# Kernel tuning notes

Measured on AMD Instinct MI355X. Metric: run time of the kernel, lower is better.

Reference implementation:

```python
import jax, jax.numpy as jnp
import numpy as np

KERNEL_SIZE = 4
SCALE = 0.5


def setup_inputs() -> dict:
    key = jax.random.key(0)
    k1, k2, k3 = jax.random.split(key, 3)
    M, K, N = 16384, 1024, 4096
    x = jax.random.normal(k1, (M, K), dtype=jnp.float32)
    weight = jax.random.normal(k2, (N, K), dtype=jnp.float32)
    bias = jax.random.normal(k3, (N,), dtype=jnp.float32)
    return {"x": x, "weight": weight, "bias": bias}


def reference(x, weight, bias):
    # y = x @ W^T + b : (M, N)
    y = jnp.einsum('mk,nk->mn', x, weight) + bias[None, :]
    M, N = y.shape
    valid_n = (N // KERNEL_SIZE) * KERNEL_SIZE
    # MaxPool1d(kernel_size, stride=kernel_size): (M, N//k, k) -> max over window
    pooled = jnp.max(y[:, :valid_n].reshape(M, valid_n // KERNEL_SIZE, KERNEL_SIZE), axis=-1)
    # sum over pooled features, then scale -> (M,)
    return jnp.sum(pooled, axis=-1) * SCALE
```

## Files before the change

### kernel.cpp

```cpp
#include <hip/hip_runtime.h>
#include <stdint.h>

#define M_DIM 16384
#define K_DIM 1024
#define N_DIM 4096
#define BM 128
#define BN 128
#define LDSP 40

#define TILE_ELEMS (128 * K_DIM)
#define SLAB_ELEMS (128 * 32)
#define NSLAB_X ((M_DIM / 128) * 32)
#define NSLAB_W ((N_DIM / 128) * 32)
#define CROW 20

typedef __bf16 bf16;
typedef __attribute__((ext_vector_type(8))) __bf16 bf16x8;
typedef __attribute__((ext_vector_type(4))) float f32x4;

__device__ __forceinline__ uint32_t pack2_bf16(float a, float b) {
    uint32_t ua = __float_as_uint(a);
    uint32_t ub = __float_as_uint(b);
    ua += 0x7fffu + ((ua >> 16) & 1u);
    ub += 0x7fffu + ((ub >> 16) & 1u);
    return (ua >> 16) | (ub & 0xffff0000u);
}

__global__ __launch_bounds__(256) void convert_pack_kernel(
    const float* __restrict__ x, const float* __restrict__ w,
    bf16* __restrict__ xp, bf16* __restrict__ wp)
{
    int slab = blockIdx.x;
    const float* src;
    bf16* dst;
    if (slab < NSLAB_X) { src = x; dst = xp; }
    else                { slab -= NSLAB_X; src = w; dst = wp; }
    const int tile = slab >> 5;
    const int s    = slab & 31;

    __shared__ uint32_t ls[128 * CROW];

    const int t = threadIdx.x;
    {
        const int r  = t >> 1;
        const int kh = (t & 1) * 16;
        const float4* p = (const float4*)(src + (size_t)(tile * 128 + r) * K_DIM + s * 32 + kh);
        float4 a = p[0], b = p[1], c = p[2], d = p[3];
        uint4* lp = (uint4*)&ls[r * CROW + (t & 1) * 8];
        uint4 v0, v1;
        v0.x = pack2_bf16(a.x, a.y); v0.y = pack2_bf16(a.z, a.w);
        v0.z = pack2_bf16(b.x, b.y); v0.w = pack2_bf16(b.z, b.w);
        v1.x = pack2_bf16(c.x, c.y); v1.y = pack2_bf16(c.z, c.w);
        v1.z = pack2_bf16(d.x, d.y); v1.w = pack2_bf16(d.z, d.w);
        lp[0] = v0; lp[1] = v1;
    }
    __syncthreads();
    uint4* dst4 = (uint4*)(dst + (size_t)tile * TILE_ELEMS + (size_t)s * SLAB_ELEMS);
    #pragma unroll
    for (int p = 0; p < 2; ++p) {
        const int c    = t + p * 256;
        const int lane = c & 63;
        const int rb   = c >> 6;
        const int q    = lane >> 4;
        const int lrow = lane & 15;
        const int r    = rb * 16 + lrow;
        const uint4* lp = (const uint4*)&ls[r * CROW + q * 4];
        dst4[c] = lp[0];
    }
}

__device__ __forceinline__ void load_set(const bf16* g, bf16x8* f) {
    #pragma unroll
    for (int i = 0; i < 4; ++i) f[i] = *(const bf16x8*)(g + i * 512);
}

__device__ __forceinline__ void do_mfma(const bf16x8* af, const bf16x8* bf,
                                        f32x4 acc[4][4]) {
    #pragma unroll
    for (int i = 0; i < 4; ++i)
        #pragma unroll
        for (int j = 0; j < 4; ++j)
            acc[i][j] = __builtin_amdgcn_mfma_f32_16x16x32_bf16(af[i], bf[j], acc[i][j], 0, 0, 0);
}

__global__ __launch_bounds__(256, 3) void gemm_pool_direct_kernel(
    const bf16* __restrict__ xp, const bf16* __restrict__ wp,
    const float* __restrict__ bias, float* __restrict__ out)
{
    const int b     = blockIdx.x;
    const int xcd   = b & 7;
    const int o     = (b >> 3) & 7;
    const int bx    = (b >> 6) & 31;
    const int phase = b >> 11;
    const int by    = phase * 64 + xcd * 8 + o;

    const int lane = threadIdx.x & 63;
    const int wave = threadIdx.x >> 6;
    const int wm = wave >> 1;
    const int wn = wave & 1;
    const int lr = lane & 15;
    const int quad = lane >> 4;

    const bf16* Abase = xp + (size_t)by * TILE_ELEMS + (wm * 4) * 512 + lane * 8;
    const bf16* Bbase = wp + (size_t)bx * TILE_ELEMS + (wn * 4) * 512 + lane * 8;

    f32x4 acc[4][4] = {};
    bf16x8 Af[2][4];
    bf16x8 Bf[3][4];

    load_set(Bbase, Bf[0]);
    load_set(Bbase + SLAB_ELEMS, Bf[1]);
    load_set(Abase, Af[0]);

    #pragma unroll
    for (int s = 0; s < 32; ++s) {
        if (s + 2 < 32) load_set(Bbase + (s + 2) * SLAB_ELEMS, Bf[(s + 2) % 3]);
        if (s + 1 < 32) load_set(Abase + (s + 1) * SLAB_ELEMS, Af[(s + 1) & 1]);
        do_mfma(Af[s & 1], Bf[s % 3], acc);
    }

    float bv[4];
    #pragma unroll
    for (int j = 0; j < 4; ++j)
        bv[j] = bias[bx * BN + wn * 64 + j * 16 + lr];

    #pragma unroll
    for (int i = 0; i < 4; ++i) {
        float rs[4] = {0.f, 0.f, 0.f, 0.f};
        #pragma unroll
        for (int j = 0; j < 4; ++j) {
            #pragma unroll
            for (int r = 0; r < 4; ++r) {
                float t = acc[i][j][r] + bv[j];
                t = fmaxf(t, __shfl_xor(t, 1, 64));
                t = fmaxf(t, __shfl_xor(t, 2, 64));
                rs[r] += t;
            }
        }
        #pragma unroll
        for (int r = 0; r < 4; ++r) {
            rs[r] += __shfl_xor(rs[r], 4, 64);
            rs[r] += __shfl_xor(rs[r], 8, 64);
        }
        if (lr == 0) {
            const int row = by * BM + wm * 64 + i * 16 + quad * 4;
            #pragma unroll
            for (int r = 0; r < 4; ++r)
                atomicAdd(&out[row + r], rs[r] * 0.5f);
        }
    }
}

__global__ __launch_bounds__(256) void fused_linear_pool_kernel(
    const float* __restrict__ x, const float* __restrict__ wt,
    const float* __restrict__ bias, float* __restrict__ out)
{
    __shared__ uint32_t sA[BM * LDSP / 2];
    __shared__ uint32_t sB[BN * LDSP / 2];

    const int tid = threadIdx.x;
    const int bx = blockIdx.x;
    const int by = blockIdx.y;

    const float* Abase = x  + (size_t)by * BM * K_DIM;
    const float* Bbase = wt + (size_t)bx * BN * K_DIM;

    const int lane = tid & 63;
    const int wave = tid >> 6;
    const int wm = wave >> 1;
    const int wn = wave & 1;
    const int lr = lane & 15;
    const int quad = lane >> 4;

    const int srow  = tid >> 2;
    const int scol  = (tid & 3) * 8;
    const int swidx = (tid & 3) * 4;

    f32x4 acc[4][4] = {};

    for (int kt = 0; kt < K_DIM; kt += 32) {
        #pragma unroll
        for (int p = 0; p < 2; ++p) {
            const int r = srow + p * 64;
            const float4* ga = (const float4*)(Abase + (size_t)r * K_DIM + kt + scol);
            const float4* gb = (const float4*)(Bbase + (size_t)r * K_DIM + kt + scol);
            float4 a0 = ga[0], a1 = ga[1], b0 = gb[0], b1 = gb[1];
            uint4 wa;
            wa.x = pack2_bf16(a0.x, a0.y); wa.y = pack2_bf16(a0.z, a0.w);
            wa.z = pack2_bf16(a1.x, a1.y); wa.w = pack2_bf16(a1.z, a1.w);
            *(uint4*)&sA[r * (LDSP / 2) + swidx] = wa;
            uint4 wbv;
            wbv.x = pack2_bf16(b0.x, b0.y); wbv.y = pack2_bf16(b0.z, b0.w);
            wbv.z = pack2_bf16(b1.x, b1.y); wbv.w = pack2_bf16(b1.z, b1.w);
            *(uint4*)&sB[r * (LDSP / 2) + swidx] = wbv;
        }
        __syncthreads();

        bf16x8 af[4], bfr[4];
        #pragma unroll
        for (int i = 0; i < 4; ++i)
            af[i] = *(const bf16x8*)((const bf16*)sA + (wm * 64 + i * 16 + lr) * LDSP + quad * 8);
        #pragma unroll
        for (int j = 0; j < 4; ++j)
            bfr[j] = *(const bf16x8*)((const bf16*)sB + (wn * 64 + j * 16 + lr) * LDSP + quad * 8);

        #pragma unroll
        for (int i = 0; i < 4; ++i)
            #pragma unroll
            for (int j = 0; j < 4; ++j)
                acc[i][j] = __builtin_amdgcn_mfma_f32_16x16x32_bf16(af[i], bfr[j], acc[i][j], 0, 0, 0);
        __syncthreads();
    }

    float bv[4];
    #pragma unroll
    for (int j = 0; j < 4; ++j)
        bv[j] = bias[bx * BN + wn * 64 + j * 16 + lr];

    #pragma unroll
    for (int i = 0; i < 4; ++i) {
        float rsum[4] = {0.f, 0.f, 0.f, 0.f};
        #pragma unroll
        for (int j = 0; j < 4; ++j) {
            #pragma unroll
            for (int r = 0; r < 4; ++r) {
                float t = acc[i][j][r] + bv[j];
                t = fmaxf(t, __shfl_xor(t, 1, 64));
                t = fmaxf(t, __shfl_xor(t, 2, 64));
                t += __shfl_xor(t, 4, 64);
                t += __shfl_xor(t, 8, 64);
                rsum[r] += t;
            }
        }
        if (lr == 0) {
            const int row = by * BM + wm * 64 + i * 16 + quad * 4;
            #pragma unroll
            for (int r = 0; r < 4; ++r)
                atomicAdd(&out[row + r], rsum[r] * 0.5f);
        }
    }
}

extern "C" void kernel_launch(void* const* d_in, const int* in_sizes, int n_in,
                              void* d_out, int out_size, void* d_ws, size_t ws_size,
                              hipStream_t stream) {
    const float* x  = (const float*)d_in[0];
    const float* wt = (const float*)d_in[1];
    const float* bs = (const float*)d_in[2];
    float* out = (float*)d_out;

    hipMemsetAsync(out, 0, (size_t)out_size * sizeof(float), stream);

    const size_t xe = (size_t)M_DIM * K_DIM;
    const size_t we = (size_t)N_DIM * K_DIM;
    const size_t need = (xe + we) * sizeof(bf16);

    if (ws_size >= need) {
        bf16* xp = (bf16*)d_ws;
        bf16* wp = xp + xe;
        convert_pack_kernel<<<NSLAB_X + NSLAB_W, 256, 0, stream>>>(x, wt, xp, wp);
        gemm_pool_direct_kernel<<<(M_DIM / BM) * (N_DIM / BN), 256, 0, stream>>>(xp, wp, bs, out);
    } else {
        dim3 grid(N_DIM / BN, M_DIM / BM);
        fused_linear_pool_kernel<<<grid, 256, 0, stream>>>(x, wt, bs, out);
    }
}
```

Measured before the change: 268.5 us.

## Fold output zeroing into pack kernel and use ping-pong register prefetch

Removes the separate memset launch by zeroing the output inside the first blocks of the convert/pack kernel. The GEMM main loop changes from a 3-deep B / 2-deep A register prefetch ring to a simple two-buffer ping-pong with 32-bit offsets. The occupancy hint rises from 3 to 4 blocks per SM. Together these aim to cut launch overhead and register pressure, at the cost of a shallower prefetch distance for the B operand, which may expose more global-load latency.

New measurement: 292.3 us. +8.9%, slower.

```diff
diff --git a/kernel.cpp b/kernel.cpp
--- a/kernel.cpp
+++ b/kernel.cpp
@@ -28,9 +28,12 @@
 
 __global__ __launch_bounds__(256) void convert_pack_kernel(
     const float* __restrict__ x, const float* __restrict__ w,
-    bf16* __restrict__ xp, bf16* __restrict__ wp)
+    bf16* __restrict__ xp, bf16* __restrict__ wp, float* __restrict__ out)
 {
     int slab = blockIdx.x;
+    const int t = threadIdx.x;
+    if (slab < (M_DIM / 256)) out[slab * 256 + t] = 0.f;
+
     const float* src;
     bf16* dst;
     if (slab < NSLAB_X) { src = x; dst = xp; }
@@ -40,7 +43,6 @@
 
     __shared__ uint32_t ls[128 * CROW];
 
-    const int t = threadIdx.x;
     {
         const int r  = t >> 1;
         const int kh = (t & 1) * 16;
@@ -69,9 +71,9 @@
     }
 }
 
-__device__ __forceinline__ void load_set(const bf16* g, bf16x8* f) {
-    #pragma unroll
-    for (int i = 0; i < 4; ++i) f[i] = *(const bf16x8*)(g + i * 512);
+__device__ __forceinline__ void load_set(const bf16* base, uint32_t off, bf16x8* f) {
+    #pragma unroll
+    for (int i = 0; i < 4; ++i) f[i] = *(const bf16x8*)(base + off + i * 512);
 }
 
 __device__ __forceinline__ void do_mfma(const bf16x8* af, const bf16x8* bf,
@@ -83,7 +85,7 @@
             acc[i][j] = __builtin_amdgcn_mfma_f32_16x16x32_bf16(af[i], bf[j], acc[i][j], 0, 0, 0);
 }
 
-__global__ __launch_bounds__(256, 3) void gemm_pool_direct_kernel(
+__global__ __launch_bounds__(256, 4) void gemm_pool_direct_kernel(
     const bf16* __restrict__ xp, const bf16* __restrict__ wp,
     const float* __restrict__ bias, float* __restrict__ out)
 {
@@ -101,22 +103,26 @@
     const int lr = lane & 15;
     const int quad = lane >> 4;
 
-    const bf16* Abase = xp + (size_t)by * TILE_ELEMS + (wm * 4) * 512 + lane * 8;
-    const bf16* Bbase = wp + (size_t)bx * TILE_ELEMS + (wn * 4) * 512 + lane * 8;
+    const bf16* Ab = xp + (size_t)by * TILE_ELEMS;
+    const bf16* Bb = wp + (size_t)bx * TILE_ELEMS;
+    const uint32_t aoff = (wm * 4) * 512 + lane * 8;
+    const uint32_t boff = (wn * 4) * 512 + lane * 8;
 
     f32x4 acc[4][4] = {};
-    bf16x8 Af[2][4];
-    bf16x8 Bf[3][4];
-
-    load_set(Bbase, Bf[0]);
-    load_set(Bbase + SLAB_ELEMS, Bf[1]);
-    load_set(Abase, Af[0]);
-
-    #pragma unroll
-    for (int s = 0; s < 32; ++s) {
-        if (s + 2 < 32) load_set(Bbase + (s + 2) * SLAB_ELEMS, Bf[(s + 2) % 3]);
-        if (s + 1 < 32) load_set(Abase + (s + 1) * SLAB_ELEMS, Af[(s + 1) & 1]);
-        do_mfma(Af[s & 1], Bf[s % 3], acc);
+    bf16x8 aA[4], bA[4], aB[4], bB[4];
+
+    load_set(Ab, aoff, aA);
+    load_set(Bb, boff, bA);
+    #pragma unroll
+    for (int s = 0; s < 32; s += 2) {
+        load_set(Ab, aoff + (s + 1) * SLAB_ELEMS, aB);
+        load_set(Bb, boff + (s + 1) * SLAB_ELEMS, bB);
+        do_mfma(aA, bA, acc);
+        if (s + 2 < 32) {
+            load_set(Ab, aoff + (s + 2) * SLAB_ELEMS, aA);
+            load_set(Bb, boff + (s + 2) * SLAB_ELEMS, bA);
+        }
+        do_mfma(aB, bB, acc);
     }
 
     float bv[4];
@@ -249,8 +255,6 @@
     const float* bs = (const float*)d_in[2];
     float* out = (float*)d_out;
 
-    hipMemsetAsync(out, 0, (size_t)out_size * sizeof(float), stream);
-
     const size_t xe = (size_t)M_DIM * K_DIM;
     const size_t we = (size_t)N_DIM * K_DIM;
     const size_t need = (xe + we) * sizeof(bf16);
@@ -258,9 +262,10 @@
     if (ws_size >= need) {
         bf16* xp = (bf16*)d_ws;
         bf16* wp = xp + xe;
-        convert_pack_kernel<<<NSLAB_X + NSLAB_W, 256, 0, stream>>>(x, wt, xp, wp);
+        convert_pack_kernel<<<NSLAB_X + NSLAB_W, 256, 0, stream>>>(x, wt, xp, wp, out);
         gemm_pool_direct_kernel<<<(M_DIM / BM) * (N_DIM / BN), 256, 0, stream>>>(xp, wp, bs, out);
     } else {
+        hipMemsetAsync(out, 0, (size_t)out_size * sizeof(float), stream);
         dim3 grid(N_DIM / BN, M_DIM / BM);
         fused_linear_pool_kernel<<<grid, 256, 0, stream>>>(x, wt, bs, out);
     }
```
